# Kernel optimization log

Measured on AMD Instinct MI355X. Metric: run time of the kernel, lower is better.

The kernel has to match this reference:

```python
import jax, jax.numpy as jnp
import numpy as np
import math

HIDDEN = 768
NUM_HEADS = 12
HEAD_DIM = HIDDEN // NUM_HEADS
EPS = 1e-05
MU_LEARNED = 0.0    # registered buffer init value (inference mode)
SIGMA_LEARNED = 1.0 # registered buffer init value (inference mode)
SCALES = (0.5, 1.0, 2.0)


def make_pe(n, d):
    # Sinusoidal positional encoding, identical to PositionalEncoding buffer.
    pos = np.arange(n, dtype=np.float32)[:, None]
    div = np.exp(np.arange(0, d, 2, dtype=np.float32) * (-math.log(10000.0) / d))
    pe = np.zeros((n, d), dtype=np.float32)
    pe[:, 0::2] = np.sin(pos * div)
    pe[:, 1::2] = np.cos(pos * div)
    return jnp.asarray(pe)


def setup_inputs() -> dict:
    key = jax.random.key(0)
    ks = jax.random.split(key, 12)
    B, C, Hh, Ww = 8, 256, 32, 32
    feat = jax.random.normal(ks[0], (B, C, Hh, Ww), jnp.float32)
    I = jax.random.uniform(ks[1], (B, 1, Hh, Ww), jnp.float32)
    sc_c = 1.0 / math.sqrt(C)
    sd = 1.0 / math.sqrt(HIDDEN)
    proj_w = jax.random.normal(ks[2], (C, HIDDEN), jnp.float32) * sc_c  # 1x1 conv as matmul
    proj_b = jnp.zeros((HIDDEN,), jnp.float32)
    wq = jax.random.normal(ks[3], (HIDDEN, HIDDEN), jnp.float32) * sd
    bq = jnp.zeros((HIDDEN,), jnp.float32)
    wk = jax.random.normal(ks[4], (HIDDEN, HIDDEN), jnp.float32) * sd
    bk = jnp.zeros((HIDDEN,), jnp.float32)
    wv = jax.random.normal(ks[5], (HIDDEN, HIDDEN), jnp.float32) * sd
    bv = jnp.zeros((HIDDEN,), jnp.float32)
    wo = jax.random.normal(ks[6], (HIDDEN, HIDDEN), jnp.float32) * sd
    bo = jnp.zeros((HIDDEN,), jnp.float32)
    lam = jnp.float32(0.5)
    return dict(feat=feat, I=I, proj_w=proj_w, proj_b=proj_b,
                wq=wq, bq=bq, wk=wk, bk=bk, wv=wv, bv=bv, wo=wo, bo=bo, lam=lam)


def reference(feat, I, proj_w, proj_b, wq, bq, wk, bk, wv, bv, wo, bo, lam):
    B, C, Hh, Ww = feat.shape
    N = Hh * Ww
    # HiddenFeatureProjection: 1x1 conv projection -> flatten -> tokens [B, N, D]
    tokens = jnp.einsum('bchw,cd->bhwd', feat, proj_w).reshape(B, N, HIDDEN) + proj_b
    tokens = tokens + make_pe(N, HIDDEN)[None]
    # GaussianWeightModule (inference path, learned buffers mu=0, sigma=1)
    G = sum(jnp.exp(-(I - MU_LEARNED) ** 2 / (2.0 * (k * SIGMA_LEARNED) ** 2 + EPS))
            for k in SCALES) / float(len(SCALES))  # [B,1,H,W]
    g = G.reshape(B, N)                              # H*W == N by construction
    bias = g[:, :, None] * g[:, None, :]             # [B, N, N] outer product
    # GaussianEnhancedAttention
    q = (tokens @ wq + bq).reshape(B, N, NUM_HEADS, HEAD_DIM).transpose(0, 2, 1, 3)
    k = (tokens @ wk + bk).reshape(B, N, NUM_HEADS, HEAD_DIM).transpose(0, 2, 1, 3)
    v = (tokens @ wv + bv).reshape(B, N, NUM_HEADS, HEAD_DIM).transpose(0, 2, 1, 3)
    scores = jnp.einsum('bhnd,bhmd->bhnm', q, k) / math.sqrt(HEAD_DIM)
    scores = scores + lam * bias[:, None, :, :]
    attn = jax.nn.softmax(scores, axis=-1)
    out = jnp.einsum('bhnm,bhmd->bhnd', attn, v).transpose(0, 2, 1, 3).reshape(B, N, HIDDEN)
    return out @ wo + bo
```

## Files before the change

kernel.cpp:

```cpp
#include <hip/hip_runtime.h>
#include <hip/hip_bf16.h>
#include <math.h>

#define HIDDEN 768
#define NHEADS 12
#define HDIM   64
#define NTOK   1024
#define BATCH  8
#define CIN    256
#define M_ALL  (BATCH * NTOK)
#define LSTR   72

typedef __hip_bfloat16 bf16;
typedef short frag8 __attribute__((ext_vector_type(8)));
typedef short s16x4 __attribute__((ext_vector_type(4)));
typedef unsigned int u32x2 __attribute__((ext_vector_type(2)));
typedef float f32x4 __attribute__((ext_vector_type(4)));

#define GL2LDS(gp, lp) \
    __builtin_amdgcn_global_load_lds((const __attribute__((address_space(1))) void*)(gp), \
                                     (__attribute__((address_space(3))) void*)(lp), 16, 0, 0)

__device__ __forceinline__ short f2bs(float x){
    union { bf16 h; short s; } u; u.h = __float2bfloat16(x); return u.s;
}

__device__ __forceinline__ float gaussw(float x){
    float x2 = x * x;
    return (__expf(-x2 / 0.50001f) + __expf(-x2 / 2.00001f) + __expf(-x2 / 8.00001f)) * (1.0f / 3.0f);
}

__global__ __launch_bounds__(256) void prep_all(
    const float* __restrict__ wq, const float* __restrict__ wk,
    const float* __restrict__ wv, const float* __restrict__ wo,
    const float* __restrict__ proj_w, const float* __restrict__ feat,
    short* __restrict__ wtqkv, short* __restrict__ wtp, short* __restrict__ featT)
{
    __shared__ short t[64][65];
    const int blk = blockIdx.x;
    const float* W; short* WT; int K, N, k0, n0;
    if (blk < 576) {
        int p = blk / 144, rem = blk % 144;
        const float* srcs[4] = {wq, wk, wv, wo};
        W = srcs[p]; WT = wtqkv + (size_t)p * HIDDEN * HIDDEN;
        K = HIDDEN; N = HIDDEN; k0 = (rem / 12) * 64; n0 = (rem % 12) * 64;
    } else if (blk < 624) {
        int rem = blk - 576;
        W = proj_w; WT = wtp;
        K = CIN; N = HIDDEN; k0 = (rem / 12) * 64; n0 = (rem % 12) * 64;
    } else {
        int rem = blk - 624;
        int b = rem / 64; rem %= 64;
        W = feat + (size_t)b * CIN * NTOK; WT = featT + (size_t)b * NTOK * CIN;
        K = CIN; N = NTOK; k0 = (rem / 16) * 64; n0 = (rem % 16) * 64;
    }
    const int tid = threadIdx.x;
    #pragma unroll
    for (int it = 0; it < 16; it++) {
        int e = tid + 256 * it;
        int kk = e / 64, nn = e % 64;
        t[kk][nn] = f2bs(W[(size_t)(k0 + kk) * N + n0 + nn]);
    }
    __syncthreads();
    #pragma unroll
    for (int it = 0; it < 16; it++) {
        int e = tid + 256 * it;
        int nn = e / 64, kk = e % 64;
        WT[(size_t)(n0 + nn) * K + k0 + kk] = t[kk][nn];
    }
}

__global__ __launch_bounds__(256) void transpose_v(
    const short* __restrict__ v, short* __restrict__ vT,
    const float* __restrict__ I, float* __restrict__ g)
{
    if (blockIdx.y == BATCH * NHEADS) {
        int idx = blockIdx.x * 512 + threadIdx.x * 2;
        g[idx]     = gaussw(I[idx]);
        g[idx + 1] = gaussw(I[idx + 1]);
        return;
    }
    __shared__ short t[64][65];
    const int nt = blockIdx.x;
    const int bh = blockIdx.y;
    const int b = bh / NHEADS, h = bh % NHEADS;
    const int tid = threadIdx.x;
    #pragma unroll
    for (int it = 0; it < 16; it++) {
        int e = tid + 256 * it;
        int rr = e / 64, cc = e % 64;
        t[rr][cc] = v[(size_t)(b * NTOK + nt * 64 + rr) * HIDDEN + h * HDIM + cc];
    }
    __syncthreads();
    #pragma unroll
    for (int it = 0; it < 16; it++) {
        int e = tid + 256 * it;
        int c2 = e / 64, r2 = e % 64;
        vT[((size_t)bh * HDIM + c2) * NTOK + nt * 64 + r2] = t[r2][c2];
    }
}

__global__ __launch_bounds__(256) void gemm_mfma128(
    const short* __restrict__ A, const short* __restrict__ WT0, long wt_z,
    const float* __restrict__ b0, const float* __restrict__ b1, const float* __restrict__ b2,
    short* o0, short* o1, short* o2, int K)
{
    __shared__ short Al[2][128 * 32];
    __shared__ short Bl[2][128 * 32];
    const int z = blockIdx.z;
    const short* WT  = WT0 + (size_t)z * wt_z;
    const float* bias = (z == 0) ? b0 : (z == 1) ? b1 : b2;
    short* outv       = (z == 0) ? o0 : (z == 1) ? o1 : o2;

    const int tid  = threadIdx.x;
    const int m0   = blockIdx.x * 128;
    const int n0   = blockIdx.y * 128;
    const int lane = tid & 63, wid = tid >> 6;
    const int wm   = (wid >> 1) * 64, wn = (wid & 1) * 64;
    const int l16  = lane & 15, quad = lane >> 4;

    const int sr  = lane >> 2;
    const int ssg = (lane & 3) ^ ((sr >> 1) & 3);
    const int fsw = (l16 >> 1) & 3;

    const f32x4 z4 = {0.f, 0.f, 0.f, 0.f};
    f32x4 acc[4][4];
    #pragma unroll
    for (int i = 0; i < 4; i++)
        #pragma unroll
        for (int j = 0; j < 4; j++) acc[i][j] = z4;

    #pragma unroll
    for (int t = 0; t < 2; t++) {
        int rbase = wid * 32 + t * 16;
        int r = rbase + sr;
        GL2LDS(A  + (size_t)(m0 + r) * K + ssg * 8, &Al[0][rbase * 32]);
        GL2LDS(WT + (size_t)(n0 + r) * K + ssg * 8, &Bl[0][rbase * 32]);
    }
    __syncthreads();

    const int NSTEP = K / 32;
    for (int ks = 0; ks < NSTEP; ks++) {
        const int cur = ks & 1;
        if (ks < NSTEP - 1) {
            int k0n = (ks + 1) * 32;
            #pragma unroll
            for (int t = 0; t < 2; t++) {
                int rbase = wid * 32 + t * 16;
                int r = rbase + sr;
                GL2LDS(A  + (size_t)(m0 + r) * K + k0n + ssg * 8, &Al[cur ^ 1][rbase * 32]);
                GL2LDS(WT + (size_t)(n0 + r) * K + k0n + ssg * 8, &Bl[cur ^ 1][rbase * 32]);
            }
        }
        frag8 af[4], bfr[4];
        #pragma unroll
        for (int i = 0; i < 4; i++)
            af[i]  = *(const frag8*)&Al[cur][(wm + i * 16 + l16) * 32 + ((quad ^ fsw) * 8)];
        #pragma unroll
        for (int j = 0; j < 4; j++)
            bfr[j] = *(const frag8*)&Bl[cur][(wn + j * 16 + l16) * 32 + ((quad ^ fsw) * 8)];
        #pragma unroll
        for (int i = 0; i < 4; i++)
            #pragma unroll
            for (int j = 0; j < 4; j++)
                acc[i][j] = __builtin_amdgcn_mfma_f32_16x16x32_bf16(af[i], bfr[j], acc[i][j], 0, 0, 0);
        __syncthreads();
    }

    #pragma unroll
    for (int i = 0; i < 4; i++) {
        #pragma unroll
        for (int r = 0; r < 4; r++) {
            int m = m0 + wm + i * 16 + quad * 4 + r;
            #pragma unroll
            for (int j = 0; j < 4; j++) {
                int col = n0 + wn + j * 16 + l16;
                outv[(size_t)m * HIDDEN + col] = f2bs(acc[i][j][r] + bias[col]);
            }
        }
    }
}

template<int MODE>
__global__ __launch_bounds__(256) void gemm_mfma64(
    const short* __restrict__ A, const short* __restrict__ WT,
    const float* __restrict__ bias, void* outv, int K)
{
    __shared__ short Al[64 * 32];
    __shared__ short Bl[128 * 32];
    const int tid  = threadIdx.x;
    const int m0   = blockIdx.x * 64;
    const int n0   = blockIdx.y * 128;
    const int lane = tid & 63, wid = tid >> 6;
    const int wn   = wid * 32;
    const int l16  = lane & 15, quad = lane >> 4;

    const int sr  = lane >> 2;
    const int ssg = (lane & 3) ^ ((sr >> 1) & 3);
    const int fsw = (l16 >> 1) & 3;

    const f32x4 z4 = {0.f, 0.f, 0.f, 0.f};
    f32x4 acc[4][2];
    #pragma unroll
    for (int i = 0; i < 4; i++)
        #pragma unroll
        for (int j = 0; j < 2; j++) acc[i][j] = z4;

    for (int k0 = 0; k0 < K; k0 += 32) {
        GL2LDS(A + (size_t)(m0 + wid * 16 + sr) * K + k0 + ssg * 8, &Al[(wid * 16) * 32]);
        #pragma unroll
        for (int t = 0; t < 2; t++) {
            int rbase = wid * 32 + t * 16;
            GL2LDS(WT + (size_t)(n0 + rbase + sr) * K + k0 + ssg * 8, &Bl[rbase * 32]);
        }
        __syncthreads();
        frag8 af[4], bfr[2];
        #pragma unroll
        for (int i = 0; i < 4; i++)
            af[i]  = *(const frag8*)&Al[(i * 16 + l16) * 32 + ((quad ^ fsw) * 8)];
        #pragma unroll
        for (int j = 0; j < 2; j++)
            bfr[j] = *(const frag8*)&Bl[(wn + j * 16 + l16) * 32 + ((quad ^ fsw) * 8)];
        #pragma unroll
        for (int i = 0; i < 4; i++)
            #pragma unroll
            for (int j = 0; j < 2; j++)
                acc[i][j] = __builtin_amdgcn_mfma_f32_16x16x32_bf16(af[i], bfr[j], acc[i][j], 0, 0, 0);
        __syncthreads();
    }

    const float kfac = -9.210340371976184f / 768.0f;
    #pragma unroll
    for (int i = 0; i < 4; i++) {
        #pragma unroll
        for (int r = 0; r < 4; r++) {
            int m = m0 + i * 16 + quad * 4 + r;
            #pragma unroll
            for (int j = 0; j < 2; j++) {
                int col = n0 + wn + j * 16 + l16;
                float val = acc[i][j][r] + bias[col];
                if (MODE == 1) {
                    int n_tok = m & (NTOK - 1);
                    float ang = (float)n_tok * expf((float)(2 * (col >> 1)) * kfac);
                    val += (col & 1) ? cosf(ang) : sinf(ang);
                }
                if (MODE == 2) ((float*)outv)[(size_t)m * HIDDEN + col] = val;
                else           ((short*)outv)[(size_t)m * HIDDEN + col] = f2bs(val);
            }
        }
    }
}

__global__ __launch_bounds__(256, 3) void attn_mfma(
    const short* __restrict__ q, const short* __restrict__ k, const short* __restrict__ vT,
    const float* __restrict__ g, const float* __restrict__ lam_p, short* __restrict__ out)
{
    __shared__ short Pl[128 * LSTR];
    __shared__ short Ks[2][64 * 64];
    __shared__ short Vt[2][64 * 64];

    const int tid  = threadIdx.x;
    const int lin  = blockIdx.x;
    const int xcd  = lin & 7, slot = lin >> 3;
    const int b    = xcd;
    const int h    = slot >> 3;
    const int qt   = slot & 7;
    const float L2E  = 1.4426950408889634f;
    const float lam2 = lam_p[0] * L2E;
    const float scl  = 0.125f * L2E;
    const int lane = tid & 63, wave = tid >> 6;
    const int l16  = lane & 15, quad = lane >> 4;

    const int sr   = lane >> 3;
    const int slin = lane & 7;
    const int ssg  = slin ^ sr;
    const int fsw  = l16 & 7;

    const size_t kb  = (size_t)b * NTOK * HIDDEN + h * HDIM;
    const size_t vtb = (size_t)(b * NHEADS + h) * HDIM * NTOK;
    const float* gk  = g + b * NTOK;

    frag8 aq[2][2];
    #pragma unroll
    for (int half = 0; half < 2; half++)
        #pragma unroll
        for (int kc = 0; kc < 2; kc++)
            aq[half][kc] = *(const frag8*)&q[(size_t)(b * NTOK + qt * 128 + wave * 32 + half * 16 + l16) * HIDDEN
                                             + h * HDIM + kc * 32 + quad * 8];
    float gq[2];
    #pragma unroll
    for (int half = 0; half < 2; half++)
        gq[half] = lam2 * gk[qt * 128 + wave * 32 + half * 16 + l16];

    #pragma unroll
    for (int t = 0; t < 2; t++) {
        int rbase = wave * 16 + t * 8;
        int r = rbase + sr;
        GL2LDS(k  + kb  + (size_t)r * HIDDEN + ssg * 8,  &Ks[0][rbase * 64]);
        GL2LDS(vT + vtb + (size_t)r * NTOK + ssg * 8,    &Vt[0][rbase * 64]);
    }
    __syncthreads();

    const f32x4 z4 = {0.f, 0.f, 0.f, 0.f};
    f32x4 o_acc[2][4];
    #pragma unroll
    for (int half = 0; half < 2; half++)
        #pragma unroll
        for (int d = 0; d < 4; d++) o_acc[half][d] = z4;
    float l_run[2] = {0.f, 0.f};

    for (int jt = 0; jt < 16; jt++) {
        const int cur = jt & 1;
        f32x4 gk4[4];
        #pragma unroll
        for (int t4 = 0; t4 < 4; t4++)
            gk4[t4] = *(const f32x4*)&gk[jt * 64 + t4 * 16 + quad * 4];
        __builtin_amdgcn_sched_barrier(0);
        if (jt < 15) {
            #pragma unroll
            for (int t = 0; t < 2; t++) {
                int rbase = wave * 16 + t * 8;
                int r = rbase + sr;
                GL2LDS(k  + kb  + (size_t)((jt + 1) * 64 + r) * HIDDEN + ssg * 8, &Ks[cur ^ 1][rbase * 64]);
                GL2LDS(vT + vtb + (size_t)r * NTOK + (jt + 1) * 64 + ssg * 8,     &Vt[cur ^ 1][rbase * 64]);
            }
        }

        float p[2][4][4];
        #pragma unroll
        for (int t4 = 0; t4 < 4; t4++) {
            frag8 ak0 = *(const frag8*)&Ks[cur][(t4 * 16 + l16) * 64 + ((quad ^ fsw) * 8)];
            frag8 ak1 = *(const frag8*)&Ks[cur][(t4 * 16 + l16) * 64 + (((quad + 4) ^ fsw) * 8)];
            #pragma unroll
            for (int half = 0; half < 2; half++) {
                f32x4 a = z4;
                a = __builtin_amdgcn_mfma_f32_16x16x32_bf16(ak0, aq[half][0], a, 0, 0, 0);
                a = __builtin_amdgcn_mfma_f32_16x16x32_bf16(ak1, aq[half][1], a, 0, 0, 0);
                #pragma unroll
                for (int r = 0; r < 4; r++) p[half][t4][r] = a[r];
            }
        }

        #pragma unroll
        for (int half = 0; half < 2; half++)
            #pragma unroll
            for (int t4 = 0; t4 < 4; t4++) {
                float e0 = exp2f(fmaf(p[half][t4][0], scl, gq[half] * gk4[t4][0]));
                float e1 = exp2f(fmaf(p[half][t4][1], scl, gq[half] * gk4[t4][1]));
                float e2 = exp2f(fmaf(p[half][t4][2], scl, gq[half] * gk4[t4][2]));
                float e3 = exp2f(fmaf(p[half][t4][3], scl, gq[half] * gk4[t4][3]));
                l_run[half] += (e0 + e1) + (e2 + e3);
                unsigned lo, hi;
                asm("v_cvt_pk_bf16_f32 %0, %1, %2" : "=v"(lo) : "v"(e0), "v"(e1));
                asm("v_cvt_pk_bf16_f32 %0, %1, %2" : "=v"(hi) : "v"(e2), "v"(e3));
                u32x2 w = {lo, hi};
                *(u32x2*)&Pl[(wave * 32 + half * 16 + l16) * LSTR + t4 * 16 + quad * 4] = w;
            }

        frag8 ap[2][2];
        #pragma unroll
        for (int half = 0; half < 2; half++)
            #pragma unroll
            for (int kc = 0; kc < 2; kc++)
                ap[half][kc] = *(const frag8*)&Pl[(wave * 32 + half * 16 + l16) * LSTR + kc * 32 + quad * 8];
        #pragma unroll
        for (int d = 0; d < 4; d++) {
            frag8 av0 = *(const frag8*)&Vt[cur][(d * 16 + l16) * 64 + ((quad ^ fsw) * 8)];
            frag8 av1 = *(const frag8*)&Vt[cur][(d * 16 + l16) * 64 + (((quad + 4) ^ fsw) * 8)];
            #pragma unroll
            for (int half = 0; half < 2; half++) {
                o_acc[half][d] = __builtin_amdgcn_mfma_f32_16x16x32_bf16(ap[half][0], av0, o_acc[half][d], 0, 0, 0);
                o_acc[half][d] = __builtin_amdgcn_mfma_f32_16x16x32_bf16(ap[half][1], av1, o_acc[half][d], 0, 0, 0);
            }
        }
        __syncthreads();
    }

    #pragma unroll
    for (int half = 0; half < 2; half++) {
        float l = l_run[half];
        l += __shfl_xor(l, 16);
        l += __shfl_xor(l, 32);
        #pragma unroll
        for (int r = 0; r < 4; r++) {
            float lq = __shfl(l, (lane & 48) | (quad * 4 + r));
            float inv_l = 1.0f / lq;
            int row = qt * 128 + wave * 32 + half * 16 + quad * 4 + r;
            #pragma unroll
            for (int d = 0; d < 4; d++)
                out[(size_t)(b * NTOK + row) * HIDDEN + h * HDIM + d * 16 + l16]
                    = f2bs(o_acc[half][d][r] * inv_l);
        }
    }
}

extern "C" void kernel_launch(void* const* d_in, const int* in_sizes, int n_in,
                              void* d_out, int out_size, void* d_ws, size_t ws_size,
                              hipStream_t stream)
{
    const float* feat   = (const float*)d_in[0];
    const float* I      = (const float*)d_in[1];
    const float* proj_w = (const float*)d_in[2];
    const float* proj_b = (const float*)d_in[3];
    const float* wq     = (const float*)d_in[4];
    const float* bq     = (const float*)d_in[5];
    const float* wk     = (const float*)d_in[6];
    const float* bk     = (const float*)d_in[7];
    const float* wv     = (const float*)d_in[8];
    const float* bv     = (const float*)d_in[9];
    const float* wo     = (const float*)d_in[10];
    const float* bo     = (const float*)d_in[11];
    const float* lam    = (const float*)d_in[12];
    float* out = (float*)d_out;

    short* wtqkv = (short*)d_ws;
    short* wto   = wtqkv + (size_t)3 * HIDDEN * HIDDEN;
    short* wtp   = wto   + (size_t)HIDDEN * HIDDEN;
    short* tokens= wtp   + (size_t)HIDDEN * CIN;
    short* qbuf  = tokens+ (size_t)M_ALL * HIDDEN;
    short* featT = qbuf;
    short* vTb   = tokens;
    short* kbuf  = (short*)d_out;
    short* vbuf  = kbuf + (size_t)M_ALL * HIDDEN;
    float* gbuf  = (float*)wtp;

    prep_all<<<1136, 256, 0, stream>>>(wq, wk, wv, wo, proj_w, feat, wtqkv, wtp, featT);
    gemm_mfma64<1><<<dim3(128, 6), 256, 0, stream>>>(featT, wtp, proj_b, tokens, CIN);
    gemm_mfma128<<<dim3(64, 6, 3), 256, 0, stream>>>(tokens, wtqkv, (long)HIDDEN * HIDDEN,
                                                     bq, bk, bv,
                                                     qbuf, kbuf, vbuf, HIDDEN);
    transpose_v<<<dim3(16, 97), 256, 0, stream>>>(vbuf, vTb, I, gbuf);
    attn_mfma<<<768, 256, 0, stream>>>(qbuf, kbuf, vTb, gbuf, lam, qbuf);
    gemm_mfma64<2><<<dim3(128, 6), 256, 0, stream>>>(qbuf, wto, bo, out, HIDDEN);
}
```

Before: 228.3 us.

## Precompute positional encoding table and overlap weight conversion with token projection GEMM

The sinusoidal positional encoding is now computed once into a table by the prep kernel, replacing per-element expf/sinf/cosf in the token-projection GEMM epilogue. The QKV/O weight transpose-and-convert blocks move out of the prep kernel and into the same launch as the token-projection GEMM, so that conversion work runs alongside the GEMM blocks. The cost is an extra 3 MB fp32 table written and then read back in the epilogue, and the mixed-role kernel carries the shared-memory footprint of both paths.

```diff
diff --git a/kernel.cpp b/kernel.cpp
--- a/kernel.cpp
+++ b/kernel.cpp
@@ -31,30 +31,35 @@
 }
 
 __global__ __launch_bounds__(256) void prep_all(
-    const float* __restrict__ wq, const float* __restrict__ wk,
-    const float* __restrict__ wv, const float* __restrict__ wo,
     const float* __restrict__ proj_w, const float* __restrict__ feat,
-    short* __restrict__ wtqkv, short* __restrict__ wtp, short* __restrict__ featT)
-{
+    short* __restrict__ wtp, short* __restrict__ featT, float* __restrict__ pe)
+{
+    const int blk = blockIdx.x;
+    const int tid = threadIdx.x;
+    if (blk >= 560) {
+        const float kfac = -9.210340371976184f / 768.0f;
+        int e0 = (blk - 560) * 3072 + tid;
+        #pragma unroll
+        for (int it = 0; it < 12; it++) {
+            int e = e0 + it * 256;
+            int n = e / 768;
+            int d = e - n * 768;
+            float ang = (float)n * expf((float)(2 * (d >> 1)) * kfac);
+            pe[e] = (d & 1) ? cosf(ang) : sinf(ang);
+        }
+        return;
+    }
     __shared__ short t[64][65];
-    const int blk = blockIdx.x;
     const float* W; short* WT; int K, N, k0, n0;
-    if (blk < 576) {
-        int p = blk / 144, rem = blk % 144;
-        const float* srcs[4] = {wq, wk, wv, wo};
-        W = srcs[p]; WT = wtqkv + (size_t)p * HIDDEN * HIDDEN;
-        K = HIDDEN; N = HIDDEN; k0 = (rem / 12) * 64; n0 = (rem % 12) * 64;
-    } else if (blk < 624) {
-        int rem = blk - 576;
+    if (blk < 48) {
         W = proj_w; WT = wtp;
-        K = CIN; N = HIDDEN; k0 = (rem / 12) * 64; n0 = (rem % 12) * 64;
+        K = CIN; N = HIDDEN; k0 = (blk / 12) * 64; n0 = (blk % 12) * 64;
     } else {
-        int rem = blk - 624;
+        int rem = blk - 48;
         int b = rem / 64; rem %= 64;
         W = feat + (size_t)b * CIN * NTOK; WT = featT + (size_t)b * NTOK * CIN;
         K = CIN; N = NTOK; k0 = (rem / 16) * 64; n0 = (rem % 16) * 64;
     }
-    const int tid = threadIdx.x;
     #pragma unroll
     for (int it = 0; it < 16; it++) {
         int e = tid + 256 * it;
@@ -67,6 +72,98 @@
         int e = tid + 256 * it;
         int nn = e / 64, kk = e % 64;
         WT[(size_t)(n0 + nn) * K + k0 + kk] = t[kk][nn];
+    }
+}
+
+__global__ __launch_bounds__(256) void tokens_wprep(
+    const short* __restrict__ A, const short* __restrict__ WT,
+    const float* __restrict__ bias, const float* __restrict__ pe,
+    short* __restrict__ outv,
+    const float* __restrict__ wq, const float* __restrict__ wk,
+    const float* __restrict__ wv, const float* __restrict__ wo,
+    short* __restrict__ wtqkv)
+{
+    const int blk = blockIdx.x;
+    const int tid = threadIdx.x;
+    if (blk >= 768) {
+        __shared__ short t[64][65];
+        int bw = blk - 768;
+        int p = bw / 144, rem = bw % 144;
+        const float* srcs[4] = {wq, wk, wv, wo};
+        const float* W = srcs[p];
+        short* WTo = wtqkv + (size_t)p * HIDDEN * HIDDEN;
+        int k0 = (rem / 12) * 64, n0 = (rem % 12) * 64;
+        #pragma unroll
+        for (int it = 0; it < 16; it++) {
+            int e = tid + 256 * it;
+            int kk = e / 64, nn = e % 64;
+            t[kk][nn] = f2bs(W[(size_t)(k0 + kk) * HIDDEN + n0 + nn]);
+        }
+        __syncthreads();
+        #pragma unroll
+        for (int it = 0; it < 16; it++) {
+            int e = tid + 256 * it;
+            int nn = e / 64, kk = e % 64;
+            WTo[(size_t)(n0 + nn) * HIDDEN + k0 + kk] = t[kk][nn];
+        }
+        return;
+    }
+    __shared__ short Al[64 * 32];
+    __shared__ short Bl[128 * 32];
+    const int m0   = (blk & 127) * 64;
+    const int n0   = (blk >> 7) * 128;
+    const int lane = tid & 63, wid = tid >> 6;
+    const int wn   = wid * 32;
+    const int l16  = lane & 15, quad = lane >> 4;
+
+    const int sr  = lane >> 2;
+    const int ssg = (lane & 3) ^ ((sr >> 1) & 3);
+    const int fsw = (l16 >> 1) & 3;
+
+    const f32x4 z4 = {0.f, 0.f, 0.f, 0.f};
+    f32x4 acc[4][2];
+    #pragma unroll
+    for (int i = 0; i < 4; i++)
+        #pragma unroll
+        for (int j = 0; j < 2; j++) acc[i][j] = z4;
+
+    const int K = CIN;
+    for (int k0 = 0; k0 < K; k0 += 32) {
+        GL2LDS(A + (size_t)(m0 + wid * 16 + sr) * K + k0 + ssg * 8, &Al[(wid * 16) * 32]);
+        #pragma unroll
+        for (int t = 0; t < 2; t++) {
+            int rbase = wid * 32 + t * 16;
+            GL2LDS(WT + (size_t)(n0 + rbase + sr) * K + k0 + ssg * 8, &Bl[rbase * 32]);
+        }
+        __syncthreads();
+        frag8 af[4], bfr[2];
+        #pragma unroll
+        for (int i = 0; i < 4; i++)
+            af[i]  = *(const frag8*)&Al[(i * 16 + l16) * 32 + ((quad ^ fsw) * 8)];
+        #pragma unroll
+        for (int j = 0; j < 2; j++)
+            bfr[j] = *(const frag8*)&Bl[(wn + j * 16 + l16) * 32 + ((quad ^ fsw) * 8)];
+        #pragma unroll
+        for (int i = 0; i < 4; i++)
+            #pragma unroll
+            for (int j = 0; j < 2; j++)
+                acc[i][j] = __builtin_amdgcn_mfma_f32_16x16x32_bf16(af[i], bfr[j], acc[i][j], 0, 0, 0);
+        __syncthreads();
+    }
+
+    #pragma unroll
+    for (int i = 0; i < 4; i++) {
+        #pragma unroll
+        for (int r = 0; r < 4; r++) {
+            int m = m0 + i * 16 + quad * 4 + r;
+            int n_tok = m & (NTOK - 1);
+            #pragma unroll
+            for (int j = 0; j < 2; j++) {
+                int col = n0 + wn + j * 16 + l16;
+                float val = acc[i][j][r] + bias[col] + pe[n_tok * HIDDEN + col];
+                outv[(size_t)m * HIDDEN + col] = f2bs(val);
+            }
+        }
     }
 }
 
@@ -181,10 +278,9 @@
     }
 }
 
-template<int MODE>
-__global__ __launch_bounds__(256) void gemm_mfma64(
+__global__ __launch_bounds__(256) void gemm_mfma64f(
     const short* __restrict__ A, const short* __restrict__ WT,
-    const float* __restrict__ bias, void* outv, int K)
+    const float* __restrict__ bias, float* __restrict__ outv, int K)
 {
     __shared__ short Al[64 * 32];
     __shared__ short Bl[128 * 32];
@@ -229,7 +325,6 @@
         __syncthreads();
     }
 
-    const float kfac = -9.210340371976184f / 768.0f;
     #pragma unroll
     for (int i = 0; i < 4; i++) {
         #pragma unroll
@@ -238,14 +333,7 @@
             #pragma unroll
             for (int j = 0; j < 2; j++) {
                 int col = n0 + wn + j * 16 + l16;
-                float val = acc[i][j][r] + bias[col];
-                if (MODE == 1) {
-                    int n_tok = m & (NTOK - 1);
-                    float ang = (float)n_tok * expf((float)(2 * (col >> 1)) * kfac);
-                    val += (col & 1) ? cosf(ang) : sinf(ang);
-                }
-                if (MODE == 2) ((float*)outv)[(size_t)m * HIDDEN + col] = val;
-                else           ((short*)outv)[(size_t)m * HIDDEN + col] = f2bs(val);
+                outv[(size_t)m * HIDDEN + col] = acc[i][j][r] + bias[col];
             }
         }
     }
@@ -419,17 +507,19 @@
     short* tokens= wtp   + (size_t)HIDDEN * CIN;
     short* qbuf  = tokens+ (size_t)M_ALL * HIDDEN;
     short* featT = qbuf;
+    float* pebuf = (float*)(qbuf + (size_t)2097152);
     short* vTb   = tokens;
     short* kbuf  = (short*)d_out;
     short* vbuf  = kbuf + (size_t)M_ALL * HIDDEN;
     float* gbuf  = (float*)wtp;
 
-    prep_all<<<1136, 256, 0, stream>>>(wq, wk, wv, wo, proj_w, feat, wtqkv, wtp, featT);
-    gemm_mfma64<1><<<dim3(128, 6), 256, 0, stream>>>(featT, wtp, proj_b, tokens, CIN);
+    prep_all<<<816, 256, 0, stream>>>(proj_w, feat, wtp, featT, pebuf);
+    tokens_wprep<<<1344, 256, 0, stream>>>(featT, wtp, proj_b, pebuf, tokens,
+                                           wq, wk, wv, wo, wtqkv);
     gemm_mfma128<<<dim3(64, 6, 3), 256, 0, stream>>>(tokens, wtqkv, (long)HIDDEN * HIDDEN,
                                                      bq, bk, bv,
                                                      qbuf, kbuf, vbuf, HIDDEN);
     transpose_v<<<dim3(16, 97), 256, 0, stream>>>(vbuf, vTb, I, gbuf);
     attn_mfma<<<768, 256, 0, stream>>>(qbuf, kbuf, vTb, gbuf, lam, qbuf);
-    gemm_mfma64<2><<<dim3(128, 6), 256, 0, stream>>>(qbuf, wto, bo, out, HIDDEN);
-}
+    gemm_mfma64f<<<dim3(128, 6), 256, 0, stream>>>(qbuf, wto, bo, out, HIDDEN);
+}
```

New measurement: 223.1 us, median of 2. -2.3%, faster.
